# Kernel tuning notes

Hardware: AMD Instinct MI355X
Metric: run time of the kernel (lower is better)

Reference implementation:

```python
import jax, jax.numpy as jnp
import numpy as np

MROPE_SECTION = [16, 24, 24]
HEAD_DIM = 128
NUM_HEADS = 16
NUM_KV_HEADS = 8
EPS = 1e-6


def rmsnorm(x, w, eps=EPS):
    xf = x.astype(jnp.float32)
    var = jnp.mean(xf * xf, axis=-1, keepdims=True)
    return (w * (xf * jax.lax.rsqrt(var + eps))).astype(x.dtype)


def rotate_half(x):
    d = x.shape[-1] // 2
    return jnp.concatenate([-x[..., d:], x[..., :d]], axis=-1)


def build_mrope(c):
    # c: [3, B, S, head_dim]; pick modality i%3 per section (non-interleaved path)
    sec = MROPE_SECTION * 2
    splits = np.cumsum(sec)[:-1]
    parts = jnp.split(c, splits, axis=-1)
    out = jnp.concatenate([p[i % 3] for i, p in enumerate(parts)], axis=-1)  # [B,S,hd]
    return out[:, None]  # unsqueeze dim 1 -> [B,1,S,hd]


def setup_inputs() -> dict:
    key = jax.random.key(0)
    ks = jax.random.split(key, 8)
    B, S, D = 2, 2048, 2048
    hd, H, KV = HEAD_DIM, NUM_HEADS, NUM_KV_HEADS
    hidden_states = jax.random.normal(ks[0], (B, S, D), jnp.float32)
    cos = jax.random.uniform(ks[1], (3, B, S, hd), jnp.float32, -1.0, 1.0)
    sin = jax.random.uniform(ks[2], (3, B, S, hd), jnp.float32, -1.0, 1.0)
    # additive causal mask [B,1,S,S]
    neg = jnp.full((S, S), -1e9, jnp.float32)
    causal = jnp.triu(neg, k=1)
    attention_mask = jnp.broadcast_to(causal[None, None], (B, 1, S, S))
    sc = 0.02
    Wq = jax.random.normal(ks[3], (D, H * hd), jnp.float32) * sc
    Wk = jax.random.normal(ks[4], (D, KV * hd), jnp.float32) * sc
    Wv = jax.random.normal(ks[5], (D, KV * hd), jnp.float32) * sc
    Wo = jax.random.normal(ks[6], (H * hd, D), jnp.float32) * sc
    q_norm_w = jnp.ones((hd,), jnp.float32)
    k_norm_w = jnp.ones((hd,), jnp.float32)
    return dict(hidden_states=hidden_states, cos=cos, sin=sin,
                attention_mask=attention_mask, Wq=Wq, Wk=Wk, Wv=Wv, Wo=Wo,
                q_norm_w=q_norm_w, k_norm_w=k_norm_w)


def reference(hidden_states, cos, sin, attention_mask, Wq, Wk, Wv, Wo, q_norm_w, k_norm_w):
    B, S, D = hidden_states.shape
    hd, H, KV = HEAD_DIM, NUM_HEADS, NUM_KV_HEADS
    groups = H // KV
    scaling = hd ** -0.5

    q = (hidden_states @ Wq).reshape(B, S, H, hd)
    k = (hidden_states @ Wk).reshape(B, S, KV, hd)
    v = (hidden_states @ Wv).reshape(B, S, KV, hd)

    q = rmsnorm(q, q_norm_w).transpose(0, 2, 1, 3)  # [B,H,S,hd]
    k = rmsnorm(k, k_norm_w).transpose(0, 2, 1, 3)  # [B,KV,S,hd]
    v = v.transpose(0, 2, 1, 3)                      # [B,KV,S,hd]

    c = build_mrope(cos)  # [B,1,S,hd]
    s = build_mrope(sin)
    q = q * c + rotate_half(q) * s
    k = k * c + rotate_half(k) * s

    # repeat_kv (GQA)
    k = jnp.repeat(k, groups, axis=1)  # [B,H,S,hd]
    v = jnp.repeat(v, groups, axis=1)

    scores = jnp.einsum('bhqd,bhkd->bhqk', q, k) * scaling + attention_mask
    attn = jax.nn.softmax(scores.astype(jnp.float32), axis=-1).astype(q.dtype)
    out = jnp.einsum('bhqk,bhkd->bqhd', attn, v).reshape(B, S, H * hd)
    return out @ Wo
```

## Files before the change

### kernel.cpp

```cpp
#include <hip/hip_runtime.h>
#include <hip/hip_bf16.h>

typedef unsigned short u16;
typedef __bf16 bf16x8 __attribute__((ext_vector_type(8)));
typedef float f32x4 __attribute__((ext_vector_type(4)));

#define B_ 2
#define S_ 2048
#define SCALE_LOG2E 0.12751743f

static __device__ __forceinline__ u16 f2bf(float f) {
    union { float f; unsigned int u; } v; v.f = f;
    unsigned int r = v.u + 0x7fffu + ((v.u >> 16) & 1u);
    return (u16)(r >> 16);
}
static __device__ __forceinline__ float bf2f(unsigned int u) {
    union { unsigned int u; float f; } v; v.u = u << 16;
    return v.f;
}

__device__ __forceinline__ void gload16(const u16* g, u16* l) {
    __builtin_amdgcn_global_load_lds(
        (const __attribute__((address_space(1))) u16*)g,
        (__attribute__((address_space(3))) u16*)l,
        16, 0, 0);
}

__global__ __launch_bounds__(256) void cast_f32_bf16(const float* __restrict__ src,
                                                     u16* __restrict__ dst, int n4) {
    int i = blockIdx.x * 256 + threadIdx.x;
    if (i >= n4) return;
    float4 v = reinterpret_cast<const float4*>(src)[i];
    ushort4 o;
    o.x = f2bf(v.x); o.y = f2bf(v.y); o.z = f2bf(v.z); o.w = f2bf(v.w);
    reinterpret_cast<ushort4*>(dst)[i] = o;
}

__global__ __launch_bounds__(256) void wtrans_all(
    const float* __restrict__ Wq, const float* __restrict__ Wk,
    const float* __restrict__ Wv, const float* __restrict__ Wo,
    u16* __restrict__ wqkvb, u16* __restrict__ wob)
{
    __shared__ float tile[32][33];
    int z = blockIdx.x;
    const float* src; u16* dst; int srs, ct, zz;
    if (z < 4096)      { src = Wq; dst = wqkvb;               srs = 2048; ct = 64; zz = z; }
    else if (z < 6144) { src = Wk; dst = wqkvb + 2048 * 2048; srs = 1024; ct = 32; zz = z - 4096; }
    else if (z < 8192) { src = Wv; dst = wqkvb + 3072 * 2048; srs = 1024; ct = 32; zz = z - 6144; }
    else               { src = Wo; dst = wob;                 srs = 2048; ct = 64; zz = z - 8192; }
    int c0 = (zz % ct) << 5, r0 = (zz / ct) << 5;
    int t = threadIdx.x, tx = t & 7, ty = t >> 3;
    float4 v = *(const float4*)&src[(size_t)(r0 + ty) * srs + c0 + 4 * tx];
    tile[ty][4 * tx + 0] = v.x; tile[ty][4 * tx + 1] = v.y;
    tile[ty][4 * tx + 2] = v.z; tile[ty][4 * tx + 3] = v.w;
    __syncthreads();
    ushort4 o;
    o.x = f2bf(tile[4 * tx + 0][ty]); o.y = f2bf(tile[4 * tx + 1][ty]);
    o.z = f2bf(tile[4 * tx + 2][ty]); o.w = f2bf(tile[4 * tx + 3][ty]);
    *(ushort4*)&dst[(size_t)(c0 + ty) * 2048 + r0 + 4 * tx] = o;
}

__global__ __launch_bounds__(256) void vtrans(const u16* __restrict__ src, u16* __restrict__ dst) {
    __shared__ u16 tile[32][36];
    int z = blockIdx.z;
    const u16* s = src + (size_t)(z >> 3) * 2048 * 4096 + 3072 + (z & 7) * 128;
    u16* d = dst + (size_t)z * 128 * 2048;
    int c0 = blockIdx.x << 5, r0 = blockIdx.y << 5;
    int t = threadIdx.x, tx = t & 7, ty = t >> 3;
    ushort4 v = *(const ushort4*)&s[(size_t)(r0 + ty) * 4096 + c0 + 4 * tx];
    tile[ty][4 * tx + 0] = v.x; tile[ty][4 * tx + 1] = v.y;
    tile[ty][4 * tx + 2] = v.z; tile[ty][4 * tx + 3] = v.w;
    __syncthreads();
    ushort4 o;
    o.x = tile[4 * tx + 0][ty]; o.y = tile[4 * tx + 1][ty];
    o.z = tile[4 * tx + 2][ty]; o.w = tile[4 * tx + 3][ty];
    *(ushort4*)&d[(size_t)(c0 + ty) * 2048 + r0 + 4 * tx] = o;
}

template<int BM, int BN, int OBF>
__global__ __launch_bounds__(256, 2) void gemm_tile(
    const u16* __restrict__ A, const u16* __restrict__ Bt,
    void* __restrict__ Cv, int M, int N, int K)
{
    constexpr int RM = BM / 32;
    constexpr int RN = BN / 32;
    constexpr int NGA = BM / 64;
    constexpr int NGB = BN / 64;
    __shared__ __align__(16) u16 As[2][BM * 32];
    __shared__ __align__(16) u16 Bs[2][BN * 32];
    int t = threadIdx.x;
    int wave = t >> 6, lane = t & 63;
    int quad = lane >> 4, l16 = lane & 15;
    int wm = (wave >> 1) * (BM / 2), wn = (wave & 1) * (BN / 2);
    int m0 = blockIdx.y * BM, n0 = blockIdx.x * BN;

    f32x4 acc[RM][RN];
#pragma unroll
    for (int i = 0; i < RM; ++i)
#pragma unroll
        for (int j = 0; j < RN; ++j)
            acc[i][j] = (f32x4){0.f, 0.f, 0.f, 0.f};

    int srow = wave * 16 + (lane >> 2);
    int sc8 = (lane & 3) << 3;
    const u16* Ap = A + (size_t)(m0 + srow) * K + sc8;
    const u16* Bp = Bt + (size_t)(n0 + srow) * K + sc8;
    size_t row64 = (size_t)64 * K;
    int lofs = (wave * 16) * 32;

#pragma unroll
    for (int g = 0; g < NGA; ++g) gload16(Ap + g * row64, &As[0][lofs + g * 64 * 32]);
#pragma unroll
    for (int g = 0; g < NGB; ++g) gload16(Bp + g * row64, &Bs[0][lofs + g * 64 * 32]);

    int it = 0;
    for (int k0 = 0; k0 < K; k0 += 32, ++it) {
        int buf = it & 1;
        __syncthreads();
        if (k0 + 32 < K) {
            u16* dA = &As[buf ^ 1][lofs];
            u16* dB = &Bs[buf ^ 1][lofs];
#pragma unroll
            for (int g = 0; g < NGA; ++g) gload16(Ap + g * row64 + k0 + 32, dA + g * 64 * 32);
#pragma unroll
            for (int g = 0; g < NGB; ++g) gload16(Bp + g * row64 + k0 + 32, dB + g * 64 * 32);
        }
        bf16x8 af[RM], bfr[RN];
#pragma unroll
        for (int i = 0; i < RM; ++i)
            af[i] = *(const bf16x8*)(&As[buf][(wm + i * 16 + l16) * 32 + quad * 8]);
#pragma unroll
        for (int j = 0; j < RN; ++j)
            bfr[j] = *(const bf16x8*)(&Bs[buf][(wn + j * 16 + l16) * 32 + quad * 8]);
#pragma unroll
        for (int i = 0; i < RM; ++i)
#pragma unroll
            for (int j = 0; j < RN; ++j)
                acc[i][j] = __builtin_amdgcn_mfma_f32_16x16x32_bf16(af[i], bfr[j], acc[i][j], 0, 0, 0);
    }

    if (OBF) {
        u16* C16 = (u16*)Cv;
#pragma unroll
        for (int i = 0; i < RM; ++i) {
            int rbase = m0 + wm + i * 16 + quad * 4;
#pragma unroll
            for (int j = 0; j < RN; ++j) {
                int col = n0 + wn + j * 16 + l16;
#pragma unroll
                for (int r = 0; r < 4; ++r)
                    C16[(size_t)(rbase + r) * N + col] = f2bf(acc[i][j][r]);
            }
        }
    } else {
        float* Cf = (float*)Cv;
#pragma unroll
        for (int i = 0; i < RM; ++i) {
            int rbase = m0 + wm + i * 16 + quad * 4;
#pragma unroll
            for (int j = 0; j < RN; ++j) {
                int col = n0 + wn + j * 16 + l16;
#pragma unroll
                for (int r = 0; r < 4; ++r)
                    Cf[(size_t)(rbase + r) * N + col] = acc[i][j][r];
            }
        }
    }
}

__global__ __launch_bounds__(256) void norm_rope(
    const u16* __restrict__ qkvb, const float* __restrict__ cosb,
    const float* __restrict__ sinb, const float* __restrict__ qw,
    const float* __restrict__ kw, u16* __restrict__ qout, u16* __restrict__ kout)
{
    int row = blockIdx.x;
    int b = row >> 11, s = row & 2047;
    int wave = threadIdx.x >> 6, lane = threadIdx.x & 63;
    int hv = blockIdx.y * 4 + wave;
    bool isq = hv < 16;
    int h = isq ? hv : hv - 16;
    const u16* src = qkvb + (size_t)row * 4096 + (isq ? h * 128 : 2048 + h * 128);
    int d0 = lane << 1;
    unsigned int xu = *(const unsigned int*)(src + d0);
    float x0 = bf2f(xu & 0xffffu), x1 = bf2f(xu >> 16);
    float ss = x0 * x0 + x1 * x1;
#pragma unroll
    for (int off = 32; off >= 1; off >>= 1) ss += __shfl_xor(ss, off);
    float rstd = rsqrtf(ss * (1.0f / 128.0f) + 1e-6f);
    const float* w = isq ? qw : kw;
    float2 wv = *(const float2*)(w + d0);
    float xn0 = x0 * rstd * wv.x;
    float xn1 = x1 * rstd * wv.y;
    float p0 = __shfl_xor(xn0, 32);
    float p1 = __shfl_xor(xn1, 32);
    float rh0 = (lane < 32) ? -p0 : p0;
    float rh1 = (lane < 32) ? -p1 : p1;
    int md = d0 < 16 ? 0 : d0 < 40 ? 1 : d0 < 64 ? 2 : d0 < 80 ? 0 : d0 < 104 ? 1 : 2;
    size_t cidx = ((size_t)md * (B_ * S_) + row) * 128 + d0;
    float2 c  = *(const float2*)(cosb + cidx);
    float2 sn = *(const float2*)(sinb + cidx);
    float fs = isq ? SCALE_LOG2E : 1.0f;
    float o0 = (xn0 * c.x + rh0 * sn.x) * fs;
    float o1 = (xn1 * c.y + rh1 * sn.y) * fs;
    size_t orow = isq ? ((size_t)(b * 16 + h) * 2048 + s) * 128
                      : ((size_t)(b * 8 + h) * 2048 + s) * 128;
    unsigned int pack = (unsigned int)f2bf(o0) | ((unsigned int)f2bf(o1) << 16);
    u16* dst = isq ? qout : kout;
    *(unsigned int*)(dst + orow + d0) = pack;
}

__global__ __launch_bounds__(256, 2) void attention(
    const u16* __restrict__ qb, const u16* __restrict__ kb,
    const u16* __restrict__ vt, u16* __restrict__ ao)
{
    __shared__ __align__(16) u16 Ks[2][64 * 128];
    __shared__ __align__(16) u16 Vs[2][128 * 64];
    __shared__ __align__(16) __bf16 Ps[4][2][16 * 64];

    int t = threadIdx.x;
    int wave = t >> 6, lane = t & 63;
    int quad = lane >> 4, l16 = lane & 15;
    int bx = blockIdx.x;
    int hi = bx >> 8, u = bx & 255;
    int q5 = u & 31;
    int qt = hi ? q5 : 31 - q5;
    int bkv = ((u >> 5) << 1) | hi;
    int b = bkv >> 3, kvh = bkv & 7;
    int q0 = qt << 6;

    bf16x8 af_q[2][4];
#pragma unroll
    for (int hh = 0; hh < 2; ++hh) {
        const u16* qsrc = qb + ((size_t)(b * 16 + kvh * 2 + hh) * 2048 + q0 + wave * 16 + l16) * 128 + quad * 8;
#pragma unroll
        for (int ks = 0; ks < 4; ++ks)
            af_q[hh][ks] = *(const bf16x8*)(qsrc + ks * 32);
    }

    const u16* kbase = kb + (size_t)bkv * 2048 * 128;
    const u16* vbase = vt + (size_t)bkv * 128 * 2048;
    const u16* kg[4]; const u16* vg[4];
    u16* kl0[4]; u16* kl1[4]; u16* vl0[4]; u16* vl1[4];
    {
        int kc = lane & 15, vc = lane & 7;
#pragma unroll
        for (int j = 0; j < 4; ++j) {
            int kr = wave * 16 + j * 4 + (lane >> 4);
            kg[j] = kbase + (size_t)kr * 128 + ((kc ^ (kr & 15)) << 3);
            int vr = wave * 32 + j * 8 + (lane >> 3);
            vg[j] = vbase + (size_t)vr * 2048 + ((vc ^ (vr & 7)) << 3);
            kl0[j] = &Ks[0][(wave * 16 + j * 4) * 128];
            kl1[j] = &Ks[1][(wave * 16 + j * 4) * 128];
            vl0[j] = &Vs[0][(wave * 32 + j * 8) * 64];
            vl1[j] = &Vs[1][(wave * 32 + j * 8) * 64];
        }
    }

    f32x4 o_acc[2][8];
    float lsum[2][4];
#pragma unroll
    for (int hh = 0; hh < 2; ++hh) {
#pragma unroll
        for (int i = 0; i < 8; ++i) o_acc[hh][i] = (f32x4){0.f, 0.f, 0.f, 0.f};
#pragma unroll
        for (int r = 0; r < 4; ++r) lsum[hh][r] = 0.f;
    }

#pragma unroll
    for (int j = 0; j < 4; ++j) { gload16(kg[j], kl0[j]); gload16(vg[j], vl0[j]); }

    for (int kt = 0; kt <= qt; ++kt) {
        int buf = kt & 1;
        __syncthreads();
        if (kt < qt) {
            size_t ko = (size_t)(kt + 1) * 64 * 128;
            int vo = (kt + 1) * 64;
            if (buf) {
#pragma unroll
                for (int j = 0; j < 4; ++j) { gload16(kg[j] + ko, kl0[j]); gload16(vg[j] + vo, vl0[j]); }
            } else {
#pragma unroll
                for (int j = 0; j < 4; ++j) { gload16(kg[j] + ko, kl1[j]); gload16(vg[j] + vo, vl1[j]); }
            }
        }
        const u16* Kb = Ks[buf];
        const u16* Vb = Vs[buf];

        f32x4 sa[2][4];
#pragma unroll
        for (int nt = 0; nt < 4; ++nt) { sa[0][nt] = (f32x4){0.f,0.f,0.f,0.f}; sa[1][nt] = (f32x4){0.f,0.f,0.f,0.f}; }
#pragma unroll
        for (int nt = 0; nt < 4; ++nt)
#pragma unroll
            for (int ks = 0; ks < 4; ++ks) {
                bf16x8 bk = *(const bf16x8*)(&Kb[(nt * 16 + l16) * 128 + ((((ks << 2) | quad) ^ l16) << 3)]);
                sa[0][nt] = __builtin_amdgcn_mfma_f32_16x16x32_bf16(af_q[0][ks], bk, sa[0][nt], 0, 0, 0);
                sa[1][nt] = __builtin_amdgcn_mfma_f32_16x16x32_bf16(af_q[1][ks], bk, sa[1][nt], 0, 0, 0);
            }

        bool diag = (kt == qt);
#pragma unroll
        for (int hh = 0; hh < 2; ++hh)
#pragma unroll
            for (int r = 0; r < 4; ++r) {
                int row = quad * 4 + r;
                int qi = wave * 16 + row;
#pragma unroll
                for (int nt = 0; nt < 4; ++nt) {
                    float pe = __builtin_amdgcn_exp2f(sa[hh][nt][r]);
                    int col = nt * 16 + l16;
                    if (diag && col > qi) pe = 0.f;
                    lsum[hh][r] += pe;
                    Ps[wave][hh][row * 64 + (col ^ ((row & 7) << 3))] = (__bf16)pe;
                }
            }

#pragma unroll
        for (int ks = 0; ks < 2; ++ks) {
            int csw = (((ks << 2) | quad) ^ (l16 & 7)) << 3;
            bf16x8 pa0 = *(const bf16x8*)(&Ps[wave][0][l16 * 64 + csw]);
            bf16x8 pa1 = *(const bf16x8*)(&Ps[wave][1][l16 * 64 + csw]);
#pragma unroll
            for (int dt = 0; dt < 8; ++dt) {
                bf16x8 vf = *(const bf16x8*)(&Vb[(dt * 16 + l16) * 64 + csw]);
                o_acc[0][dt] = __builtin_amdgcn_mfma_f32_16x16x32_bf16(pa0, vf, o_acc[0][dt], 0, 0, 0);
                o_acc[1][dt] = __builtin_amdgcn_mfma_f32_16x16x32_bf16(pa1, vf, o_acc[1][dt], 0, 0, 0);
            }
        }
    }

#pragma unroll
    for (int hh = 0; hh < 2; ++hh) {
#pragma unroll
        for (int r = 0; r < 4; ++r)
#pragma unroll
            for (int off = 1; off < 16; off <<= 1) lsum[hh][r] += __shfl_xor(lsum[hh][r], off);
        size_t obase = (((size_t)b * 2048 + q0 + wave * 16) * 16 + (kvh * 2 + hh)) * 128;
#pragma unroll
        for (int r = 0; r < 4; ++r) {
            float inv = 1.0f / lsum[hh][r];
            int qrow = quad * 4 + r;
#pragma unroll
            for (int dt = 0; dt < 8; ++dt)
                ao[obase + (size_t)qrow * 2048 + dt * 16 + l16] = f2bf(o_acc[hh][dt][r] * inv);
        }
    }
}

extern "C" void kernel_launch(void* const* d_in, const int* in_sizes, int n_in,
                              void* d_out, int out_size, void* d_ws, size_t ws_size,
                              hipStream_t stream) {
    const float* hs   = (const float*)d_in[0];
    const float* cosb = (const float*)d_in[1];
    const float* sinb = (const float*)d_in[2];
    const float* Wq = (const float*)d_in[4];
    const float* Wk = (const float*)d_in[5];
    const float* Wv = (const float*)d_in[6];
    const float* Wo = (const float*)d_in[7];
    const float* qw = (const float*)d_in[8];
    const float* kw = (const float*)d_in[9];
    float* out = (float*)d_out;

    char* ws = (char*)d_ws;
    u16* hsb   = (u16*)(ws);
    u16* wqkvb = (u16*)(ws + 16777216);
    u16* wob   = (u16*)(ws + 33554432);
    u16* qkvb  = (u16*)(ws + 41943040);
    u16* qb    = (u16*)(ws + 75497472);
    u16* kb    = (u16*)(ws + 92274688);
    u16* vb    = (u16*)(ws + 100663296);
    u16* aob   = (u16*)(ws + 109051904);

    cast_f32_bf16<<<8192, 256, 0, stream>>>(hs, hsb, 2097152);
    wtrans_all<<<12288, 256, 0, stream>>>(Wq, Wk, Wv, Wo, wqkvb, wob);

    gemm_tile<256, 128, 1><<<dim3(32, 16), 256, 0, stream>>>(hsb, wqkvb, qkvb, 4096, 4096, 2048);

    norm_rope<<<dim3(4096, 6), 256, 0, stream>>>(qkvb, cosb, sinb, qw, kw, qb, kb);
    vtrans<<<dim3(4, 64, 16), 256, 0, stream>>>(qkvb, vb);

    attention<<<512, 256, 0, stream>>>(qb, kb, vb, aob);

    gemm_tile<256, 128, 0><<<dim3(16, 16), 256, 0, stream>>>(aob, wob, out, 4096, 2048, 2048);
}
```

Before: 387.1 us.

## Fuse RMSNorm and mRoPE into QKV GEMM epilogue and merge prep kernels

Moves the q/k RMSNorm and mRoPE into the QKV GEMM epilogue. The warp tiling changes so each wave owns a full 128-wide head row (4 waves × 64 rows, full BN). V is written to a compact buffer before transposition, and the hidden-state cast is merged with the weight transpose into a single prep launch. This removes the intermediate bf16 QKV round trip, the norm_rope kernel and one launch. In exchange the epilogue does strided scalar cos/sin loads and 2-byte stores, and the new wave tiling loads more B fragments per wave.

New measurement: 388.5 us. Within noise of the previous version (+0.3%).

```diff
diff --git a/kernel.cpp b/kernel.cpp
--- a/kernel.cpp
+++ b/kernel.cpp
@@ -13,10 +13,6 @@
     union { float f; unsigned int u; } v; v.f = f;
     unsigned int r = v.u + 0x7fffu + ((v.u >> 16) & 1u);
     return (u16)(r >> 16);
-}
-static __device__ __forceinline__ float bf2f(unsigned int u) {
-    union { unsigned int u; float f; } v; v.u = u << 16;
-    return v.f;
 }
 
 __device__ __forceinline__ void gload16(const u16* g, u16* l) {
@@ -26,23 +22,23 @@
         16, 0, 0);
 }
 
-__global__ __launch_bounds__(256) void cast_f32_bf16(const float* __restrict__ src,
-                                                     u16* __restrict__ dst, int n4) {
-    int i = blockIdx.x * 256 + threadIdx.x;
-    if (i >= n4) return;
-    float4 v = reinterpret_cast<const float4*>(src)[i];
-    ushort4 o;
-    o.x = f2bf(v.x); o.y = f2bf(v.y); o.z = f2bf(v.z); o.w = f2bf(v.w);
-    reinterpret_cast<ushort4*>(dst)[i] = o;
-}
-
-__global__ __launch_bounds__(256) void wtrans_all(
-    const float* __restrict__ Wq, const float* __restrict__ Wk,
-    const float* __restrict__ Wv, const float* __restrict__ Wo,
+__global__ __launch_bounds__(256) void prep(
+    const float* __restrict__ hs, const float* __restrict__ Wq,
+    const float* __restrict__ Wk, const float* __restrict__ Wv,
+    const float* __restrict__ Wo, u16* __restrict__ hsb,
     u16* __restrict__ wqkvb, u16* __restrict__ wob)
 {
     __shared__ float tile[32][33];
     int z = blockIdx.x;
+    if (z < 8192) {
+        int i = z * 256 + threadIdx.x;
+        float4 v = reinterpret_cast<const float4*>(hs)[i];
+        ushort4 o;
+        o.x = f2bf(v.x); o.y = f2bf(v.y); o.z = f2bf(v.z); o.w = f2bf(v.w);
+        reinterpret_cast<ushort4*>(hsb)[i] = o;
+        return;
+    }
+    z -= 8192;
     const float* src; u16* dst; int srs, ct, zz;
     if (z < 4096)      { src = Wq; dst = wqkvb;               srs = 2048; ct = 64; zz = z; }
     else if (z < 6144) { src = Wk; dst = wqkvb + 2048 * 2048; srs = 1024; ct = 32; zz = z - 4096; }
@@ -60,14 +56,14 @@
     *(ushort4*)&dst[(size_t)(c0 + ty) * 2048 + r0 + 4 * tx] = o;
 }
 
-__global__ __launch_bounds__(256) void vtrans(const u16* __restrict__ src, u16* __restrict__ dst) {
+__global__ __launch_bounds__(256) void vtrans(const u16* __restrict__ vsrc, u16* __restrict__ dst) {
     __shared__ u16 tile[32][36];
     int z = blockIdx.z;
-    const u16* s = src + (size_t)(z >> 3) * 2048 * 4096 + 3072 + (z & 7) * 128;
+    const u16* s = vsrc + (size_t)(z >> 3) * 2048 * 1024 + (z & 7) * 128;
     u16* d = dst + (size_t)z * 128 * 2048;
     int c0 = blockIdx.x << 5, r0 = blockIdx.y << 5;
     int t = threadIdx.x, tx = t & 7, ty = t >> 3;
-    ushort4 v = *(const ushort4*)&s[(size_t)(r0 + ty) * 4096 + c0 + 4 * tx];
+    ushort4 v = *(const ushort4*)&s[(size_t)(r0 + ty) * 1024 + c0 + 4 * tx];
     tile[ty][4 * tx + 0] = v.x; tile[ty][4 * tx + 1] = v.y;
     tile[ty][4 * tx + 2] = v.z; tile[ty][4 * tx + 3] = v.w;
     __syncthreads();
@@ -77,21 +73,21 @@
     *(ushort4*)&d[(size_t)(c0 + ty) * 2048 + r0 + 4 * tx] = o;
 }
 
-template<int BM, int BN, int OBF>
-__global__ __launch_bounds__(256, 2) void gemm_tile(
-    const u16* __restrict__ A, const u16* __restrict__ Bt,
-    void* __restrict__ Cv, int M, int N, int K)
+template<int EPI>
+__global__ __launch_bounds__(256, 2) void gemm_qkv(
+    const u16* __restrict__ A, const u16* __restrict__ Bt, float* __restrict__ Cf,
+    u16* __restrict__ qb, u16* __restrict__ kb, u16* __restrict__ vsrc,
+    const float* __restrict__ cosb, const float* __restrict__ sinb,
+    const float* __restrict__ qw, const float* __restrict__ kw,
+    int M, int N, int K)
 {
-    constexpr int RM = BM / 32;
-    constexpr int RN = BN / 32;
-    constexpr int NGA = BM / 64;
-    constexpr int NGB = BN / 64;
+    constexpr int BM = 256, BN = 128, RM = 4, RN = 8;
     __shared__ __align__(16) u16 As[2][BM * 32];
     __shared__ __align__(16) u16 Bs[2][BN * 32];
     int t = threadIdx.x;
     int wave = t >> 6, lane = t & 63;
     int quad = lane >> 4, l16 = lane & 15;
-    int wm = (wave >> 1) * (BM / 2), wn = (wave & 1) * (BN / 2);
+    int wm = wave * 64;
     int m0 = blockIdx.y * BM, n0 = blockIdx.x * BN;
 
     f32x4 acc[RM][RN];
@@ -109,9 +105,9 @@
     int lofs = (wave * 16) * 32;
 
 #pragma unroll
-    for (int g = 0; g < NGA; ++g) gload16(Ap + g * row64, &As[0][lofs + g * 64 * 32]);
-#pragma unroll
-    for (int g = 0; g < NGB; ++g) gload16(Bp + g * row64, &Bs[0][lofs + g * 64 * 32]);
+    for (int g = 0; g < 4; ++g) gload16(Ap + g * row64, &As[0][lofs + g * 64 * 32]);
+#pragma unroll
+    for (int g = 0; g < 2; ++g) gload16(Bp + g * row64, &Bs[0][lofs + g * 64 * 32]);
 
     int it = 0;
     for (int k0 = 0; k0 < K; k0 += 32, ++it) {
@@ -121,9 +117,9 @@
             u16* dA = &As[buf ^ 1][lofs];
             u16* dB = &Bs[buf ^ 1][lofs];
 #pragma unroll
-            for (int g = 0; g < NGA; ++g) gload16(Ap + g * row64 + k0 + 32, dA + g * 64 * 32);
-#pragma unroll
-            for (int g = 0; g < NGB; ++g) gload16(Bp + g * row64 + k0 + 32, dB + g * 64 * 32);
+            for (int g = 0; g < 4; ++g) gload16(Ap + g * row64 + k0 + 32, dA + g * 64 * 32);
+#pragma unroll
+            for (int g = 0; g < 2; ++g) gload16(Bp + g * row64 + k0 + 32, dB + g * 64 * 32);
         }
         bf16x8 af[RM], bfr[RN];
 #pragma unroll
@@ -131,7 +127,7 @@
             af[i] = *(const bf16x8*)(&As[buf][(wm + i * 16 + l16) * 32 + quad * 8]);
 #pragma unroll
         for (int j = 0; j < RN; ++j)
-            bfr[j] = *(const bf16x8*)(&Bs[buf][(wn + j * 16 + l16) * 32 + quad * 8]);
+            bfr[j] = *(const bf16x8*)(&Bs[buf][(j * 16 + l16) * 32 + quad * 8]);
 #pragma unroll
         for (int i = 0; i < RM; ++i)
 #pragma unroll
@@ -139,74 +135,70 @@
                 acc[i][j] = __builtin_amdgcn_mfma_f32_16x16x32_bf16(af[i], bfr[j], acc[i][j], 0, 0, 0);
     }
 
-    if (OBF) {
-        u16* C16 = (u16*)Cv;
+    if (EPI == 0) {
 #pragma unroll
         for (int i = 0; i < RM; ++i) {
             int rbase = m0 + wm + i * 16 + quad * 4;
 #pragma unroll
             for (int j = 0; j < RN; ++j) {
-                int col = n0 + wn + j * 16 + l16;
-#pragma unroll
-                for (int r = 0; r < 4; ++r)
-                    C16[(size_t)(rbase + r) * N + col] = f2bf(acc[i][j][r]);
-            }
-        }
-    } else {
-        float* Cf = (float*)Cv;
-#pragma unroll
-        for (int i = 0; i < RM; ++i) {
-            int rbase = m0 + wm + i * 16 + quad * 4;
-#pragma unroll
-            for (int j = 0; j < RN; ++j) {
-                int col = n0 + wn + j * 16 + l16;
+                int col = n0 + j * 16 + l16;
 #pragma unroll
                 for (int r = 0; r < 4; ++r)
                     Cf[(size_t)(rbase + r) * N + col] = acc[i][j][r];
             }
         }
-    }
-}
-
-__global__ __launch_bounds__(256) void norm_rope(
-    const u16* __restrict__ qkvb, const float* __restrict__ cosb,
-    const float* __restrict__ sinb, const float* __restrict__ qw,
-    const float* __restrict__ kw, u16* __restrict__ qout, u16* __restrict__ kout)
-{
-    int row = blockIdx.x;
-    int b = row >> 11, s = row & 2047;
-    int wave = threadIdx.x >> 6, lane = threadIdx.x & 63;
-    int hv = blockIdx.y * 4 + wave;
-    bool isq = hv < 16;
-    int h = isq ? hv : hv - 16;
-    const u16* src = qkvb + (size_t)row * 4096 + (isq ? h * 128 : 2048 + h * 128);
-    int d0 = lane << 1;
-    unsigned int xu = *(const unsigned int*)(src + d0);
-    float x0 = bf2f(xu & 0xffffu), x1 = bf2f(xu >> 16);
-    float ss = x0 * x0 + x1 * x1;
-#pragma unroll
-    for (int off = 32; off >= 1; off >>= 1) ss += __shfl_xor(ss, off);
-    float rstd = rsqrtf(ss * (1.0f / 128.0f) + 1e-6f);
-    const float* w = isq ? qw : kw;
-    float2 wv = *(const float2*)(w + d0);
-    float xn0 = x0 * rstd * wv.x;
-    float xn1 = x1 * rstd * wv.y;
-    float p0 = __shfl_xor(xn0, 32);
-    float p1 = __shfl_xor(xn1, 32);
-    float rh0 = (lane < 32) ? -p0 : p0;
-    float rh1 = (lane < 32) ? -p1 : p1;
-    int md = d0 < 16 ? 0 : d0 < 40 ? 1 : d0 < 64 ? 2 : d0 < 80 ? 0 : d0 < 104 ? 1 : 2;
-    size_t cidx = ((size_t)md * (B_ * S_) + row) * 128 + d0;
-    float2 c  = *(const float2*)(cosb + cidx);
-    float2 sn = *(const float2*)(sinb + cidx);
-    float fs = isq ? SCALE_LOG2E : 1.0f;
-    float o0 = (xn0 * c.x + rh0 * sn.x) * fs;
-    float o1 = (xn1 * c.y + rh1 * sn.y) * fs;
-    size_t orow = isq ? ((size_t)(b * 16 + h) * 2048 + s) * 128
-                      : ((size_t)(b * 8 + h) * 2048 + s) * 128;
-    unsigned int pack = (unsigned int)f2bf(o0) | ((unsigned int)f2bf(o1) << 16);
-    u16* dst = isq ? qout : kout;
-    *(unsigned int*)(dst + orow + d0) = pack;
+    } else {
+        int hblk = n0 >> 7;
+        if (hblk < 24) {
+            bool isq = hblk < 16;
+            const float* wptr = isq ? qw : kw;
+            float wv[8];
+#pragma unroll
+            for (int j = 0; j < 8; ++j) wv[j] = wptr[j * 16 + l16];
+            u16* dbase = isq ? qb + ((size_t)hblk * 2048) * 128
+                             : kb + ((size_t)(hblk - 16) * 2048) * 128;
+            size_t bstride = isq ? (size_t)16 * 2048 * 128 : (size_t)8 * 2048 * 128;
+#pragma unroll
+            for (int i = 0; i < RM; ++i) {
+#pragma unroll
+                for (int r = 0; r < 4; ++r) {
+                    float x[8], ss = 0.f;
+#pragma unroll
+                    for (int j = 0; j < 8; ++j) { x[j] = acc[i][j][r]; ss += x[j] * x[j]; }
+#pragma unroll
+                    for (int off = 1; off < 16; off <<= 1) ss += __shfl_xor(ss, off);
+                    float rstd = rsqrtf(ss * (1.0f / 128.0f) + 1e-6f);
+                    int m = m0 + wm + i * 16 + quad * 4 + r;
+                    float xn[8];
+#pragma unroll
+                    for (int j = 0; j < 8; ++j) xn[j] = x[j] * rstd * wv[j];
+                    u16* dst = dbase + (size_t)(m >> 11) * bstride + (size_t)(m & 2047) * 128;
+#pragma unroll
+                    for (int j = 0; j < 8; ++j) {
+                        int c = j * 16 + l16;
+                        float rh = (j < 4) ? -xn[j ^ 4] : xn[j ^ 4];
+                        int md = c < 16 ? 0 : c < 40 ? 1 : c < 64 ? 2 : c < 80 ? 0 : c < 104 ? 1 : 2;
+                        size_t ci = ((size_t)md * (B_ * S_) + m) * 128 + c;
+                        float o = xn[j] * cosb[ci] + rh * sinb[ci];
+                        if (isq) o *= SCALE_LOG2E;
+                        dst[c] = f2bf(o);
+                    }
+                }
+            }
+        } else {
+            int vcol0 = (hblk - 24) * 128;
+#pragma unroll
+            for (int i = 0; i < RM; ++i) {
+#pragma unroll
+                for (int r = 0; r < 4; ++r) {
+                    int m = m0 + wm + i * 16 + quad * 4 + r;
+#pragma unroll
+                    for (int j = 0; j < RN; ++j)
+                        vsrc[(size_t)m * 1024 + vcol0 + j * 16 + l16] = f2bf(acc[i][j][r]);
+                }
+            }
+        }
+    }
 }
 
 __global__ __launch_bounds__(256, 2) void attention(
@@ -365,21 +357,21 @@
     u16* hsb   = (u16*)(ws);
     u16* wqkvb = (u16*)(ws + 16777216);
     u16* wob   = (u16*)(ws + 33554432);
-    u16* qkvb  = (u16*)(ws + 41943040);
-    u16* qb    = (u16*)(ws + 75497472);
-    u16* kb    = (u16*)(ws + 92274688);
-    u16* vb    = (u16*)(ws + 100663296);
-    u16* aob   = (u16*)(ws + 109051904);
-
-    cast_f32_bf16<<<8192, 256, 0, stream>>>(hs, hsb, 2097152);
-    wtrans_all<<<12288, 256, 0, stream>>>(Wq, Wk, Wv, Wo, wqkvb, wob);
-
-    gemm_tile<256, 128, 1><<<dim3(32, 16), 256, 0, stream>>>(hsb, wqkvb, qkvb, 4096, 4096, 2048);
-
-    norm_rope<<<dim3(4096, 6), 256, 0, stream>>>(qkvb, cosb, sinb, qw, kw, qb, kb);
-    vtrans<<<dim3(4, 64, 16), 256, 0, stream>>>(qkvb, vb);
+    u16* qb    = (u16*)(ws + 41943040);
+    u16* kb    = (u16*)(ws + 58720256);
+    u16* vsrc  = (u16*)(ws + 67108864);
+    u16* vb    = (u16*)(ws + 75497472);
+    u16* aob   = (u16*)(ws + 83886080);
+
+    prep<<<20480, 256, 0, stream>>>(hs, Wq, Wk, Wv, Wo, hsb, wqkvb, wob);
+
+    gemm_qkv<1><<<dim3(32, 16), 256, 0, stream>>>(hsb, wqkvb, nullptr,
+        qb, kb, vsrc, cosb, sinb, qw, kw, 4096, 4096, 2048);
+
+    vtrans<<<dim3(4, 64, 16), 256, 0, stream>>>(vsrc, vb);
 
     attention<<<512, 256, 0, stream>>>(qb, kb, vb, aob);
 
-    gemm_tile<256, 128, 0><<<dim3(16, 16), 256, 0, stream>>>(aob, wob, out, 4096, 2048, 2048);
-}
+    gemm_qkv<0><<<dim3(16, 16), 256, 0, stream>>>(aob, wob, out,
+        nullptr, nullptr, nullptr, nullptr, nullptr, nullptr, nullptr, 4096, 2048, 2048);
+}
```
